# Performance work log

Hardware: AMD Instinct MI355X
Metric: run time of the kernel (lower is better)

## Reference

```python
import jax, jax.numpy as jnp
import numpy as np

NUM_LAYER = 5
HIDDEN = 128
PROJ = 256
ATOM_VOCAB = 128
BOND_VOCAB = 16
N_ATOM_FEATS = 9
N_BOND_FEATS = 3
BN_EPS = 1e-5


def _batchnorm(x, gamma, beta):
    # training-mode BatchNorm1d over the node axis
    mu = x.mean(axis=0)
    var = x.var(axis=0)
    return (x - mu) * jax.lax.rsqrt(var + BN_EPS) * gamma + beta


def setup_inputs() -> dict:
    key = jax.random.key(0)
    ks = jax.random.split(key, 16)
    N, E = 40000, 640000
    s = 0.05
    inp = {
        "x": jax.random.randint(ks[0], (N, N_ATOM_FEATS), 0, ATOM_VOCAB, dtype=jnp.int32),
        "edge_index": jax.random.randint(ks[1], (2, E), 0, N, dtype=jnp.int32),
        "edge_attr": jax.random.randint(ks[2], (E, N_BOND_FEATS), 0, BOND_VOCAB, dtype=jnp.int32),
        "atom_emb": jax.random.normal(ks[3], (N_ATOM_FEATS, ATOM_VOCAB, HIDDEN), jnp.float32) * s,
        "bond_emb": jax.random.normal(ks[4], (NUM_LAYER, N_BOND_FEATS, BOND_VOCAB, HIDDEN), jnp.float32) * s,
        "eps": jnp.zeros((NUM_LAYER,), jnp.float32),
        "w1": jax.random.normal(ks[5], (NUM_LAYER, HIDDEN, 2 * HIDDEN), jnp.float32) * s,
        "b1": jnp.zeros((NUM_LAYER, 2 * HIDDEN), jnp.float32),
        "bn1_g": jnp.ones((NUM_LAYER, 2 * HIDDEN), jnp.float32),
        "bn1_b": jnp.zeros((NUM_LAYER, 2 * HIDDEN), jnp.float32),
        "w2": jax.random.normal(ks[6], (NUM_LAYER, 2 * HIDDEN, HIDDEN), jnp.float32) * s,
        "b2": jnp.zeros((NUM_LAYER, HIDDEN), jnp.float32),
        "bn_g": jnp.ones((NUM_LAYER, HIDDEN), jnp.float32),
        "bn_b": jnp.zeros((NUM_LAYER, HIDDEN), jnp.float32),
        "lin_w": jax.random.normal(ks[7], (HIDDEN, PROJ), jnp.float32) * s,
        "lin_b": jnp.zeros((PROJ,), jnp.float32),
    }
    return inp


def reference(x, edge_index, edge_attr, atom_emb, bond_emb, eps, w1, b1, bn1_g, bn1_b, w2, b2, bn_g, bn_b, lin_w, lin_b):
    N = x.shape[0]
    src, dst = edge_index[0], edge_index[1]
    # AtomEncoder: sum of per-column embeddings -> [N, H]
    h = atom_emb[jnp.arange(N_ATOM_FEATS), x].sum(axis=1)
    for l in range(NUM_LAYER):
        # BondEncoder for this layer -> [E, H]
        e = bond_emb[l][jnp.arange(N_BOND_FEATS), edge_attr].sum(axis=1)
        # message: relu(x_j + edge_emb); aggregate: scatter-add to dst
        msg = jax.nn.relu(h[src] + e)
        agg = jax.ops.segment_sum(msg, dst, num_segments=N)
        z = (1.0 + eps[l]) * h + agg
        # GIN MLP: Linear -> BN -> ReLU -> Linear
        z = z @ w1[l] + b1[l]
        z = jax.nn.relu(_batchnorm(z, bn1_g[l], bn1_b[l]))
        z = z @ w2[l] + b2[l]
        # outer BatchNorm, relu except last layer
        h = _batchnorm(z, bn_g[l], bn_b[l])
        if l < NUM_LAYER - 1:
            h = jax.nn.relu(h)
    return h @ lin_w + lin_b
```

## Files before the change

### kernel.cpp

```cpp
#include <hip/hip_runtime.h>
#include <stdint.h>


typedef unsigned short ushort_t;
typedef unsigned int uint_t;
typedef __attribute__((ext_vector_type(8))) short bf16x8;
typedef __attribute__((ext_vector_type(16))) float f32x16;

#define MFMA32(a, b, c) __builtin_amdgcn_mfma_f32_32x32x16_bf16(a, b, c, 0, 0, 0)

__device__ inline ushort_t f2bf(float f) {
  uint_t u = __builtin_bit_cast(uint_t, f);
  u += 0x7FFFu + ((u >> 16) & 1u);
  return (ushort_t)(u >> 16);
}
__device__ inline float bf2f(uint_t h) {
  uint_t u = (h & 0xFFFFu) << 16;
  return __builtin_bit_cast(float, u);
}
__device__ inline uint_t pack2(float a, float b) {
  return (uint_t)f2bf(a) | ((uint_t)f2bf(b) << 16);
}
__device__ inline f32x16 zero16() {
  f32x16 z;
#pragma unroll
  for (int i = 0; i < 16; ++i) z[i] = 0.f;
  return z;
}


__global__ __launch_bounds__(256) void bond_comb_k(
    const float* __restrict__ bemb, ushort_t* __restrict__ comb)
{
  int idx = blockIdx.x * 256 + threadIdx.x;
  if (idx >= 5 * 4096 * 64) return;
  int lane = idx & 63, c = (idx >> 6) & 4095, l = idx >> 18;
  const float2* b2 = (const float2*)(bemb + (size_t)l * 3 * 16 * 128);
  float2 e0 = b2[(c & 15) * 64 + lane];
  float2 e1 = b2[(16 + ((c >> 4) & 15)) * 64 + lane];
  float2 e2 = b2[(32 + (c >> 8)) * 64 + lane];
  ((uint_t*)comb)[idx] = pack2(e0.x + e1.x + e2.x, e0.y + e1.y + e2.y);
}

__global__ __launch_bounds__(256) void swz_all_k(
    const float* __restrict__ w1, const float* __restrict__ linw,
    const float* __restrict__ w2, ushort_t* __restrict__ bswz1,
    ushort_t* __restrict__ bswz2)
{
  int t = blockIdx.x * 256 + threadIdx.x;
  if (t >= 11 * 4096) return;
  int m = t >> 12, tt = t & 4095, lane = tt & 63;
  if (m < 6) {
    const float* w = (m < 5) ? (w1 + (size_t)m * 32768) : linw;
    ushort_t* o = bswz1 + (size_t)m * 32768;
    int nt = (tt >> 6) & 7, s = tt >> 9;
    int kb = s * 16 + (lane >> 5) * 8, n = nt * 32 + (lane & 31);
    ushort_t tmp[8];
#pragma unroll
    for (int j = 0; j < 8; ++j) tmp[j] = f2bf(w[(size_t)(kb + j) * 256 + n]);
    ((uint4*)o)[tt] = *(uint4*)tmp;
  } else {
    int mm = m - 6;
    const float* w = w2 + (size_t)mm * 32768;
    ushort_t* o = bswz2 + (size_t)mm * 32768;
    int nt = (tt >> 6) & 3, s = tt >> 8;
    int kb = s * 16 + (lane >> 5) * 8, n = nt * 32 + (lane & 31);
    ushort_t tmp[8];
#pragma unroll
    for (int j = 0; j < 8; ++j) tmp[j] = f2bf(w[(size_t)(kb + j) * 128 + n]);
    ((uint4*)o)[tt] = *(uint4*)tmp;
  }
}


__global__ void zero_int_k(int* p, int n) {
  int i = blockIdx.x * 256 + threadIdx.x;
  if (i < n) p[i] = 0;
}

__global__ void hist_k(const int* __restrict__ ei, int* __restrict__ cnt, int E) {
  int e = blockIdx.x * 256 + threadIdx.x;
  if (e >= E) return;
  atomicAdd(&cnt[ei[E + e]], 1);
}

__global__ __launch_bounds__(256) void block_sum_k(
    const int* __restrict__ cnt, int* __restrict__ bsum, int N)
{
  __shared__ int red[256];
  int t = threadIdx.x, idx = blockIdx.x * 256 + t;
  red[t] = (idx < N) ? cnt[idx] : 0;
  __syncthreads();
  for (int o = 128; o > 0; o >>= 1) {
    if (t < o) red[t] += red[t + o];
    __syncthreads();
  }
  if (t == 0) bsum[blockIdx.x] = red[0];
}

__global__ __launch_bounds__(256) void scan_bsum_k(
    int* __restrict__ bsum, int* __restrict__ rsN, int nb)
{
  __shared__ int s[256];
  int t = threadIdx.x;
  s[t] = (t < nb) ? bsum[t] : 0;
  __syncthreads();
  for (int o = 1; o < 256; o <<= 1) {
    int v = (t >= o) ? s[t - o] : 0;
    __syncthreads();
    s[t] += v;
    __syncthreads();
  }
  if (t < nb) bsum[t] = (t == 0) ? 0 : s[t - 1];
  if (t == nb - 1) *rsN = s[t];
}

__global__ __launch_bounds__(256) void scan_write_k(
    const int* __restrict__ cnt, const int* __restrict__ bsum,
    int* __restrict__ rs, int* __restrict__ cursor, int N)
{
  __shared__ int s[256];
  int t = threadIdx.x, idx = blockIdx.x * 256 + t;
  int v = (idx < N) ? cnt[idx] : 0;
  s[t] = v;
  __syncthreads();
  for (int o = 1; o < 256; o <<= 1) {
    int u = (t >= o) ? s[t - o] : 0;
    __syncthreads();
    s[t] += u;
    __syncthreads();
  }
  int excl = s[t] - v + bsum[blockIdx.x];
  if (idx < N) { rs[idx] = excl; cursor[idx] = excl; }
}

__global__ void scatter_k(const int* __restrict__ ei, const int* __restrict__ ea,
                          int* __restrict__ cursor, uint32_t* __restrict__ sorted, int E)
{
  int e = blockIdx.x * 256 + threadIdx.x;
  if (e >= E) return;
  int src = ei[e], dst = ei[E + e];
  int a0 = ea[e * 3], a1 = ea[e * 3 + 1], a2 = ea[e * 3 + 2];
  int pos = atomicAdd(&cursor[dst], 1);
  sorted[pos] = (uint32_t)src | ((uint32_t)a0 << 16) | ((uint32_t)a1 << 20) | ((uint32_t)a2 << 24);
}


__global__ __launch_bounds__(256) void atom_encode_k(
    const int* __restrict__ x, const float* __restrict__ aemb,
    ushort_t* __restrict__ hbn, float* __restrict__ stats, int N)
{
  if (blockIdx.x == 0) {
    stats[threadIdx.x] = 0.f;
    stats[threadIdx.x + 256] = 0.f;
  }
  int idx = blockIdx.x * 256 + threadIdx.x;
  if (idx >= N * 64) return;
  int n = idx >> 6, lane = idx & 63;
  const int* xr = x + n * 9;
  float sx = 0.f, sy = 0.f;
#pragma unroll
  for (int f = 0; f < 9; ++f) {
    float2 e = ((const float2*)(aemb + (size_t)(f * 128 + xr[f]) * 128))[lane];
    sx += e.x; sy += e.y;
  }
  ((uint_t*)hbn)[idx] = pack2(sx, sy);
}

__global__ __launch_bounds__(256) void bnrelu_k(
    const float* __restrict__ raw, const float* __restrict__ stats2,
    const float* __restrict__ g, const float* __restrict__ bb,
    ushort_t* __restrict__ hbn, float* __restrict__ statsZero,
    float invN, int total)
{
  if (blockIdx.x == 0) {
    statsZero[threadIdx.x] = 0.f;
    statsZero[threadIdx.x + 256] = 0.f;
  }
  int t = blockIdx.x * 256 + threadIdx.x;
  int lane = t & 63;
  int c0 = 2 * lane, c1 = c0 + 1;
  float mu0 = stats2[c0] * invN, mu1 = stats2[c1] * invN;
  float v0 = stats2[128 + c0] * invN - mu0 * mu0;
  float v1 = stats2[128 + c1] * invN - mu1 * mu1;
  float scx = rsqrtf(v0 + 1e-5f) * g[c0];
  float scy = rsqrtf(v1 + 1e-5f) * g[c1];
  float shx = bb[c0] - mu0 * scx;
  float shy = bb[c1] - mu1 * scy;
  int stride = gridDim.x * 256;
  for (int idx = t; idx < total; idx += stride) {
    float2 h = ((const float2*)raw)[idx];
    float hx = fmaxf(fmaf(h.x, scx, shx), 0.f);
    float hy = fmaxf(fmaf(h.y, scy, shy), 0.f);
    ((uint_t*)hbn)[idx] = pack2(hx, hy);
  }
}

__global__ __launch_bounds__(512, 4) void agg_gemm1_k(
    const ushort_t* __restrict__ hbn, const ushort_t* __restrict__ comb,
    const uint32_t* __restrict__ sorted, const int* __restrict__ rs,
    const float* __restrict__ eps, int layer,
    const ushort_t* __restrict__ bswz, const float* __restrict__ bias,
    ushort_t* __restrict__ z1bf, float* __restrict__ stats, int N)
{
  __shared__ ushort_t As[64 * 128];
  __shared__ ushort_t Al[64 * 128];
  int tid = threadIdx.x;
  int wave = tid >> 6, lane = tid & 63;
  int row0 = blockIdx.x * 64;
  if (blockIdx.x == 0 && tid < 256) stats[512 + tid] = 0.f;
  const uint_t* hb = (const uint_t*)hbn;
  const uint_t* cb = ((const uint_t*)comb) + (size_t)layer * 4096 * 64;
  float s_eps = 1.f + eps[layer];
#pragma unroll 1
  for (int j = 0; j < 8; ++j) {
    int r = wave + 8 * j;
    int n = row0 + r;
    int beg = rs[n], end = rs[n + 1];
    float ax = 0.f, ay = 0.f;
    int i = beg;
    for (; i + 16 <= end; i += 16) {
      uint32_t p[16];
#pragma unroll
      for (int jj = 0; jj < 16; ++jj) p[jj] = sorted[i + jj];
      uint_t hv[16], ee[16];
#pragma unroll
      for (int jj = 0; jj < 16; ++jj) {
        hv[jj] = hb[(size_t)(p[jj] & 0xFFFFu) * 64 + lane];
        ee[jj] = cb[(p[jj] >> 16) * 64 + lane];
      }
#pragma unroll
      for (int jj = 0; jj < 16; ++jj) {
        ax += fmaxf(bf2f(hv[jj]) + bf2f(ee[jj]), 0.f);
        ay += fmaxf(bf2f(hv[jj] >> 16) + bf2f(ee[jj] >> 16), 0.f);
      }
    }
    for (; i + 4 <= end; i += 4) {
      uint32_t p[4];
#pragma unroll
      for (int jj = 0; jj < 4; ++jj) p[jj] = sorted[i + jj];
      uint_t hv[4], ee[4];
#pragma unroll
      for (int jj = 0; jj < 4; ++jj) {
        hv[jj] = hb[(size_t)(p[jj] & 0xFFFFu) * 64 + lane];
        ee[jj] = cb[(p[jj] >> 16) * 64 + lane];
      }
#pragma unroll
      for (int jj = 0; jj < 4; ++jj) {
        ax += fmaxf(bf2f(hv[jj]) + bf2f(ee[jj]), 0.f);
        ay += fmaxf(bf2f(hv[jj] >> 16) + bf2f(ee[jj] >> 16), 0.f);
      }
    }
    for (; i < end; ++i) {
      uint32_t p = sorted[i];
      uint_t ee = cb[(p >> 16) * 64 + lane];
      uint_t hv = hb[(size_t)(p & 0xFFFFu) * 64 + lane];
      ax += fmaxf(bf2f(hv) + bf2f(ee), 0.f);
      ay += fmaxf(bf2f(hv >> 16) + bf2f(ee >> 16), 0.f);
    }
    uint_t hn = hb[(size_t)n * 64 + lane];
    float zx = fmaf(s_eps, bf2f(hn), ax);
    float zy = fmaf(s_eps, bf2f(hn >> 16), ay);
    ushort_t hxz = f2bf(zx), hyz = f2bf(zy);
    float lox = zx - bf2f(hxz), loy = zy - bf2f(hyz);
    int c = 2 * lane;
    int scol = (((c >> 3) ^ (r & 15)) << 3) | (c & 7);
    *(uint_t*)&As[r * 128 + scol] = (uint_t)hxz | ((uint_t)hyz << 16);
    *(uint_t*)&Al[r * 128 + scol] = pack2(lox, loy);
  }
  __syncthreads();
  int lr = lane & 31, half = lane >> 5;
  int nt = wave;
  f32x16 acc0 = zero16(), acc1 = zero16();
  const bf16x8* Bp = (const bf16x8*)bswz;
#pragma unroll
  for (int s = 0; s < 8; ++s) {
    int k = s * 16 + half * 8;
    int scol = ((k >> 3) ^ (lr & 15)) << 3;
    bf16x8 b = Bp[(s * 8 + nt) * 64 + lane];
    bf16x8 ah0 = *(const bf16x8*)&As[lr * 128 + scol];
    bf16x8 al0 = *(const bf16x8*)&Al[lr * 128 + scol];
    bf16x8 ah1 = *(const bf16x8*)&As[(32 + lr) * 128 + scol];
    bf16x8 al1 = *(const bf16x8*)&Al[(32 + lr) * 128 + scol];
    acc0 = MFMA32(ah0, b, acc0);
    acc0 = MFMA32(al0, b, acc0);
    acc1 = MFMA32(ah1, b, acc1);
    acc1 = MFMA32(al1, b, acc1);
  }
  int col = nt * 32 + lr;
  float bv = bias[col];
  float s0 = 0.f, q0 = 0.f;
#pragma unroll
  for (int r2 = 0; r2 < 16; ++r2) {
    int rrow = (r2 & 3) + 8 * (r2 >> 2) + 4 * half;
    float v0 = acc0[r2] + bv;
    float v1 = acc1[r2] + bv;
    z1bf[(size_t)(row0 + rrow) * 256 + col] = f2bf(v0);
    z1bf[(size_t)(row0 + 32 + rrow) * 256 + col] = f2bf(v1);
    s0 += v0 + v1;
    q0 += v0 * v0 + v1 * v1;
  }
  s0 += __shfl_xor(s0, 32);
  q0 += __shfl_xor(q0, 32);
  if (lane < 32) {
    atomicAdd(&stats[col], s0);
    atomicAdd(&stats[256 + col], q0);
  }
}

__global__ __launch_bounds__(256) void mlp2_k(
    float* rawz, const float* __restrict__ stats1,
    const float* __restrict__ g1, const float* __restrict__ bb1,
    const ushort_t* __restrict__ bswz2, const float* __restrict__ b2,
    float* __restrict__ stats2, float invN)
{
  __shared__ ushort_t Bs[64 * 256];
  __shared__ float sc1[256], sh1[256];
  int tid = threadIdx.x;
  int wave = tid >> 6, lane = tid & 63;
  int lr = lane & 31, half = lane >> 5;
  int row0 = blockIdx.x * 64;
  {
    float mu = stats1[tid] * invN;
    float var = stats1[256 + tid] * invN - mu * mu;
    float r = rsqrtf(var + 1e-5f) * g1[tid];
    sc1[tid] = r;
    sh1[tid] = bb1[tid] - mu * r;
  }
  __syncthreads();
  {
    const uint4* src = (const uint4*)((const ushort_t*)rawz + (size_t)row0 * 256);
#pragma unroll
    for (int i = 0; i < 8; ++i) {
      int idx = tid + 256 * i;
      int r = idx >> 5, c = (idx & 31) * 8;
      uint4 v = src[idx];
      float f0 = fmaxf(fmaf(bf2f(v.x), sc1[c], sh1[c]), 0.f);
      float f1 = fmaxf(fmaf(bf2f(v.x >> 16), sc1[c + 1], sh1[c + 1]), 0.f);
      float f2 = fmaxf(fmaf(bf2f(v.y), sc1[c + 2], sh1[c + 2]), 0.f);
      float f3 = fmaxf(fmaf(bf2f(v.y >> 16), sc1[c + 3], sh1[c + 3]), 0.f);
      float f4 = fmaxf(fmaf(bf2f(v.z), sc1[c + 4], sh1[c + 4]), 0.f);
      float f5 = fmaxf(fmaf(bf2f(v.z >> 16), sc1[c + 5], sh1[c + 5]), 0.f);
      float f6 = fmaxf(fmaf(bf2f(v.w), sc1[c + 6], sh1[c + 6]), 0.f);
      float f7 = fmaxf(fmaf(bf2f(v.w >> 16), sc1[c + 7], sh1[c + 7]), 0.f);
      uint4 o;
      o.x = pack2(f0, f1);
      o.y = pack2(f2, f3);
      o.z = pack2(f4, f5);
      o.w = pack2(f6, f7);
      int scol = ((c >> 3) ^ (r & 15)) << 3;
      *(uint4*)&Bs[r * 256 + scol] = o;
    }
  }
  __syncthreads();
  f32x16 acc0 = zero16(), acc1 = zero16();
  {
    const bf16x8* Bp2 = (const bf16x8*)bswz2;
#pragma unroll
    for (int s = 0; s < 16; ++s) {
      int k = s * 16 + half * 8;
      int scol = ((k >> 3) ^ (lr & 15)) << 3;
      bf16x8 a0 = *(const bf16x8*)&Bs[lr * 256 + scol];
      bf16x8 a1 = *(const bf16x8*)&Bs[(32 + lr) * 256 + scol];
      bf16x8 b = Bp2[(s * 4 + wave) * 64 + lane];
      acc0 = MFMA32(a0, b, acc0);
      acc1 = MFMA32(a1, b, acc1);
    }
  }
  int col = wave * 32 + lr;
  float bv = b2[col];
  float s0 = 0.f, q0 = 0.f;
  auto emit = [&](const f32x16& a, int mtb) {
#pragma unroll
    for (int r2 = 0; r2 < 16; ++r2) {
      int row = row0 + mtb + (r2 & 3) + 8 * (r2 >> 2) + 4 * half;
      float v = a[r2] + bv;
      rawz[(size_t)row * 128 + col] = v;
      s0 += v;
      q0 += v * v;
    }
  };
  emit(acc0, 0);
  emit(acc1, 32);
  s0 += __shfl_xor(s0, 32);
  q0 += __shfl_xor(q0, 32);
  if (lane < 32) {
    atomicAdd(&stats2[col], s0);
    atomicAdd(&stats2[128 + col], q0);
  }
}

__global__ __launch_bounds__(256) void final_proj_k(
    const float* __restrict__ inf, const ushort_t* __restrict__ bswz,
    const float* __restrict__ bias, const float* __restrict__ stats2,
    const float* __restrict__ g, const float* __restrict__ bb,
    float* __restrict__ outf, float invN)
{
  __shared__ ushort_t As[64 * 128];
  __shared__ float sc[128], sh[128];
  int tid = threadIdx.x;
  int wave = tid >> 6, lane = tid & 63;
  int lr = lane & 31, half = lane >> 5;
  int row0 = blockIdx.x * 64;
  if (tid < 128) {
    int c = tid;
    float mu = stats2[c] * invN;
    float var = stats2[128 + c] * invN - mu * mu;
    float r = rsqrtf(var + 1e-5f) * g[c];
    sc[c] = r;
    sh[c] = bb[c] - mu * r;
  }
  __syncthreads();
  {
    const float4* src = (const float4*)(inf + (size_t)row0 * 128);
#pragma unroll
    for (int i = 0; i < 8; ++i) {
      int idx = tid + 256 * i;
      int r = idx >> 5, c = (idx & 31) * 4;
      float4 v = src[idx];
      v.x = fmaf(v.x, sc[c], sh[c]);
      v.y = fmaf(v.y, sc[c + 1], sh[c + 1]);
      v.z = fmaf(v.z, sc[c + 2], sh[c + 2]);
      v.w = fmaf(v.w, sc[c + 3], sh[c + 3]);
      uint2 o;
      o.x = pack2(v.x, v.y);
      o.y = pack2(v.z, v.w);
      int scol = (((c >> 3) ^ (r & 15)) << 3) | (c & 7);
      *(uint2*)&As[r * 128 + scol] = o;
    }
  }
  __syncthreads();
  int nt0 = wave * 2, nt1 = nt0 + 1;
  f32x16 acc00 = zero16(), acc01 = zero16(), acc10 = zero16(), acc11 = zero16();
  const bf16x8* Bp = (const bf16x8*)bswz;
#pragma unroll
  for (int s = 0; s < 8; ++s) {
    int k = s * 16 + half * 8;
    int scol = ((k >> 3) ^ (lr & 15)) << 3;
    bf16x8 a0 = *(const bf16x8*)&As[lr * 128 + scol];
    bf16x8 a1 = *(const bf16x8*)&As[(32 + lr) * 128 + scol];
    bf16x8 b0 = Bp[(s * 8 + nt0) * 64 + lane];
    bf16x8 b1 = Bp[(s * 8 + nt1) * 64 + lane];
    acc00 = MFMA32(a0, b0, acc00);
    acc10 = MFMA32(a1, b0, acc10);
    acc01 = MFMA32(a0, b1, acc01);
    acc11 = MFMA32(a1, b1, acc11);
  }
  int col0 = nt0 * 32 + lr, col1 = nt1 * 32 + lr;
  float bv0 = bias[col0], bv1 = bias[col1];
  auto emit = [&](const f32x16& a, int mtb, int col, float bv) {
#pragma unroll
    for (int r2 = 0; r2 < 16; ++r2) {
      int row = row0 + mtb + (r2 & 3) + 8 * (r2 >> 2) + 4 * half;
      outf[(size_t)row * 256 + col] = a[r2] + bv;
    }
  };
  emit(acc00, 0, col0, bv0);
  emit(acc10, 32, col0, bv0);
  emit(acc01, 0, col1, bv1);
  emit(acc11, 32, col1, bv1);
}

extern "C" void kernel_launch(void* const* d_in, const int* in_sizes, int n_in,
                              void* d_out, int out_size, void* d_ws, size_t ws_size,
                              hipStream_t stream)
{
  const int* x = (const int*)d_in[0];
  const int* ei = (const int*)d_in[1];
  const int* ea = (const int*)d_in[2];
  const float* aemb = (const float*)d_in[3];
  const float* bemb = (const float*)d_in[4];
  const float* eps = (const float*)d_in[5];
  const float* w1 = (const float*)d_in[6];
  const float* b1 = (const float*)d_in[7];
  const float* bn1g = (const float*)d_in[8];
  const float* bn1b = (const float*)d_in[9];
  const float* w2 = (const float*)d_in[10];
  const float* b2 = (const float*)d_in[11];
  const float* bng = (const float*)d_in[12];
  const float* bnb = (const float*)d_in[13];
  const float* linw = (const float*)d_in[14];
  const float* linb = (const float*)d_in[15];
  int N = in_sizes[0] / 9;
  int E = in_sizes[1] / 2;
  int nb = (N + 255) / 256;

  char* ws = (char*)d_ws;
  size_t off = 0;
  auto alloc = [&](size_t bytes) {
    void* p = ws + off;
    off += (bytes + 255) & ~(size_t)255;
    return p;
  };
  float* raw = (float*)alloc((size_t)N * 128 * 4);
  ushort_t* hbn = (ushort_t*)alloc((size_t)N * 128 * 2);
  ushort_t* comb = (ushort_t*)alloc((size_t)5 * 4096 * 128 * 2);
  ushort_t* bswz1 = (ushort_t*)alloc((size_t)6 * 32768 * 2);
  ushort_t* bswz2 = (ushort_t*)alloc((size_t)5 * 32768 * 2);
  uint32_t* sorted = (uint32_t*)alloc((size_t)E * 4);
  int* rs = (int*)alloc((size_t)(N + 1) * 4);
  int* cursor = (int*)alloc((size_t)N * 4);
  int* cnt = (int*)alloc((size_t)N * 4);
  int* bsum = (int*)alloc((size_t)nb * 4);
  float* stats = (float*)alloc(768 * 4);
  float invN = 1.f / (float)N;

  bond_comb_k<<<(5 * 4096 * 64 + 255) / 256, 256, 0, stream>>>(bemb, comb);
  swz_all_k<<<(11 * 4096 + 255) / 256, 256, 0, stream>>>(w1, linw, w2, bswz1, bswz2);

  atom_encode_k<<<(N * 64 + 255) / 256, 256, 0, stream>>>(x, aemb, hbn, stats, N);
  zero_int_k<<<(N + 255) / 256, 256, 0, stream>>>(cnt, N);
  hist_k<<<(E + 255) / 256, 256, 0, stream>>>(ei, cnt, E);
  block_sum_k<<<nb, 256, 0, stream>>>(cnt, bsum, N);
  scan_bsum_k<<<1, 256, 0, stream>>>(bsum, rs + N, nb);
  scan_write_k<<<nb, 256, 0, stream>>>(cnt, bsum, rs, cursor, N);
  scatter_k<<<(E + 255) / 256, 256, 0, stream>>>(ei, ea, cursor, sorted, E);

  for (int l = 0; l < 5; ++l) {
    if (l > 0) {
      bnrelu_k<<<2048, 256, 0, stream>>>(
          raw, stats + 512, bng + (size_t)(l - 1) * 128,
          bnb + (size_t)(l - 1) * 128, hbn, stats, invN, N * 64);
    }
    agg_gemm1_k<<<N / 64, 512, 0, stream>>>(
        hbn, comb, sorted, rs, eps, l,
        bswz1 + (size_t)l * 32768, b1 + (size_t)l * 256,
        (ushort_t*)raw, stats, N);
    mlp2_k<<<N / 64, 256, 0, stream>>>(
        raw, stats, bn1g + (size_t)l * 256, bn1b + (size_t)l * 256,
        bswz2 + (size_t)l * 32768, b2 + (size_t)l * 128,
        stats + 512, invN);
  }
  final_proj_k<<<N / 64, 256, 0, stream>>>(
      raw, bswz1 + (size_t)5 * 32768, linb, stats + 512,
      bng + (size_t)4 * 128, bnb + (size_t)4 * 128, (float*)d_out, invN);
}
```

Measured before the change: 622.7 us.

## Split fused aggregate+GEMM1 kernel into separate aggregation and GEMM kernels

```diff
diff --git a/kernel.cpp b/kernel.cpp
--- a/kernel.cpp
+++ b/kernel.cpp
@@ -196,12 +196,74 @@
   }
 }
 
-__global__ __launch_bounds__(512, 4) void agg_gemm1_k(
+__global__ __launch_bounds__(256) void aggregate_k(
     const ushort_t* __restrict__ hbn, const ushort_t* __restrict__ comb,
     const uint32_t* __restrict__ sorted, const int* __restrict__ rs,
-    const float* __restrict__ eps, int layer,
-    const ushort_t* __restrict__ bswz, const float* __restrict__ bias,
-    ushort_t* __restrict__ z1bf, float* __restrict__ stats, int N)
+    const float* __restrict__ eps, int layer, uint2* zinout, int N)
+{
+  int wave = threadIdx.x >> 6, lane = threadIdx.x & 63;
+  int n = blockIdx.x * 4 + wave;
+  if (n >= N) return;
+  int beg = rs[n], end = rs[n + 1];
+  const uint_t* hb = (const uint_t*)hbn;
+  const uint_t* cb = ((const uint_t*)comb) + (size_t)layer * 4096 * 64;
+  float ax = 0.f, ay = 0.f;
+  int i = beg;
+  for (; i + 16 <= end; i += 16) {
+    uint32_t p[16];
+#pragma unroll
+    for (int j = 0; j < 16; ++j) p[j] = sorted[i + j];
+    uint_t hv[16], ee[16];
+#pragma unroll
+    for (int j = 0; j < 16; ++j) {
+      hv[j] = hb[(size_t)(p[j] & 0xFFFFu) * 64 + lane];
+      ee[j] = cb[(p[j] >> 16) * 64 + lane];
+    }
+#pragma unroll
+    for (int j = 0; j < 16; ++j) {
+      ax += fmaxf(bf2f(hv[j]) + bf2f(ee[j]), 0.f);
+      ay += fmaxf(bf2f(hv[j] >> 16) + bf2f(ee[j] >> 16), 0.f);
+    }
+  }
+  for (; i + 4 <= end; i += 4) {
+    uint32_t p[4];
+#pragma unroll
+    for (int j = 0; j < 4; ++j) p[j] = sorted[i + j];
+    uint_t hv[4], ee[4];
+#pragma unroll
+    for (int j = 0; j < 4; ++j) {
+      hv[j] = hb[(size_t)(p[j] & 0xFFFFu) * 64 + lane];
+      ee[j] = cb[(p[j] >> 16) * 64 + lane];
+    }
+#pragma unroll
+    for (int j = 0; j < 4; ++j) {
+      ax += fmaxf(bf2f(hv[j]) + bf2f(ee[j]), 0.f);
+      ay += fmaxf(bf2f(hv[j] >> 16) + bf2f(ee[j] >> 16), 0.f);
+    }
+  }
+  for (; i < end; ++i) {
+    uint32_t p = sorted[i];
+    uint_t ee = cb[(p >> 16) * 64 + lane];
+    uint_t hv = hb[(size_t)(p & 0xFFFFu) * 64 + lane];
+    ax += fmaxf(bf2f(hv) + bf2f(ee), 0.f);
+    ay += fmaxf(bf2f(hv >> 16) + bf2f(ee >> 16), 0.f);
+  }
+  float s = 1.f + eps[layer];
+  uint_t hn = hb[(size_t)n * 64 + lane];
+  float zx = fmaf(s, bf2f(hn), ax);
+  float zy = fmaf(s, bf2f(hn >> 16), ay);
+  ushort_t hxz = f2bf(zx), hyz = f2bf(zy);
+  float lox = zx - bf2f(hxz), loy = zy - bf2f(hyz);
+  uint2 o;
+  o.x = (uint_t)hxz | ((uint_t)hyz << 16);
+  o.y = pack2(lox, loy);
+  zinout[(size_t)n * 64 + lane] = o;
+}
+
+__global__ __launch_bounds__(512, 4) void gemm1_k(
+    const uint2* zin, const ushort_t* __restrict__ bswz,
+    const float* __restrict__ bias, ushort_t* z1bf,
+    float* __restrict__ stats)
 {
   __shared__ ushort_t As[64 * 128];
   __shared__ ushort_t Al[64 * 128];
@@ -209,64 +271,17 @@
   int wave = tid >> 6, lane = tid & 63;
   int row0 = blockIdx.x * 64;
   if (blockIdx.x == 0 && tid < 256) stats[512 + tid] = 0.f;
-  const uint_t* hb = (const uint_t*)hbn;
-  const uint_t* cb = ((const uint_t*)comb) + (size_t)layer * 4096 * 64;
-  float s_eps = 1.f + eps[layer];
-#pragma unroll 1
-  for (int j = 0; j < 8; ++j) {
-    int r = wave + 8 * j;
-    int n = row0 + r;
-    int beg = rs[n], end = rs[n + 1];
-    float ax = 0.f, ay = 0.f;
-    int i = beg;
-    for (; i + 16 <= end; i += 16) {
-      uint32_t p[16];
-#pragma unroll
-      for (int jj = 0; jj < 16; ++jj) p[jj] = sorted[i + jj];
-      uint_t hv[16], ee[16];
-#pragma unroll
-      for (int jj = 0; jj < 16; ++jj) {
-        hv[jj] = hb[(size_t)(p[jj] & 0xFFFFu) * 64 + lane];
-        ee[jj] = cb[(p[jj] >> 16) * 64 + lane];
-      }
-#pragma unroll
-      for (int jj = 0; jj < 16; ++jj) {
-        ax += fmaxf(bf2f(hv[jj]) + bf2f(ee[jj]), 0.f);
-        ay += fmaxf(bf2f(hv[jj] >> 16) + bf2f(ee[jj] >> 16), 0.f);
-      }
-    }
-    for (; i + 4 <= end; i += 4) {
-      uint32_t p[4];
-#pragma unroll
-      for (int jj = 0; jj < 4; ++jj) p[jj] = sorted[i + jj];
-      uint_t hv[4], ee[4];
-#pragma unroll
-      for (int jj = 0; jj < 4; ++jj) {
-        hv[jj] = hb[(size_t)(p[jj] & 0xFFFFu) * 64 + lane];
-        ee[jj] = cb[(p[jj] >> 16) * 64 + lane];
-      }
-#pragma unroll
-      for (int jj = 0; jj < 4; ++jj) {
-        ax += fmaxf(bf2f(hv[jj]) + bf2f(ee[jj]), 0.f);
-        ay += fmaxf(bf2f(hv[jj] >> 16) + bf2f(ee[jj] >> 16), 0.f);
-      }
-    }
-    for (; i < end; ++i) {
-      uint32_t p = sorted[i];
-      uint_t ee = cb[(p >> 16) * 64 + lane];
-      uint_t hv = hb[(size_t)(p & 0xFFFFu) * 64 + lane];
-      ax += fmaxf(bf2f(hv) + bf2f(ee), 0.f);
-      ay += fmaxf(bf2f(hv >> 16) + bf2f(ee >> 16), 0.f);
-    }
-    uint_t hn = hb[(size_t)n * 64 + lane];
-    float zx = fmaf(s_eps, bf2f(hn), ax);
-    float zy = fmaf(s_eps, bf2f(hn >> 16), ay);
-    ushort_t hxz = f2bf(zx), hyz = f2bf(zy);
-    float lox = zx - bf2f(hxz), loy = zy - bf2f(hyz);
-    int c = 2 * lane;
-    int scol = (((c >> 3) ^ (r & 15)) << 3) | (c & 7);
-    *(uint_t*)&As[r * 128 + scol] = (uint_t)hxz | ((uint_t)hyz << 16);
-    *(uint_t*)&Al[r * 128 + scol] = pack2(lox, loy);
+  {
+    const uint2* src = zin + (size_t)row0 * 64;
+#pragma unroll
+    for (int i = 0; i < 8; ++i) {
+      int idx = tid + 512 * i;
+      int r = idx >> 6, l = idx & 63, c = 2 * l;
+      uint2 v = src[idx];
+      int scol = (((c >> 3) ^ (r & 15)) << 3) | (c & 7);
+      *(uint_t*)&As[r * 128 + scol] = v.x;
+      *(uint_t*)&Al[r * 128 + scol] = v.y;
+    }
   }
   __syncthreads();
   int lr = lane & 31, half = lane >> 5;
@@ -522,10 +537,11 @@
           raw, stats + 512, bng + (size_t)(l - 1) * 128,
           bnb + (size_t)(l - 1) * 128, hbn, stats, invN, N * 64);
     }
-    agg_gemm1_k<<<N / 64, 512, 0, stream>>>(
-        hbn, comb, sorted, rs, eps, l,
-        bswz1 + (size_t)l * 32768, b1 + (size_t)l * 256,
-        (ushort_t*)raw, stats, N);
+    aggregate_k<<<(N + 3) / 4, 256, 0, stream>>>(
+        hbn, comb, sorted, rs, eps, l, (uint2*)raw, N);
+    gemm1_k<<<N / 64, 512, 0, stream>>>(
+        (const uint2*)raw, bswz1 + (size_t)l * 32768, b1 + (size_t)l * 256,
+        (ushort_t*)raw, stats);
     mlp2_k<<<N / 64, 256, 0, stream>>>(
         raw, stats, bn1g + (size_t)l * 256, bn1b + (size_t)l * 256,
         bswz2 + (size_t)l * 32768, b2 + (size_t)l * 128,
```

New measurement: 635.3 us. 2.0% more time.
